# Optimization experiments

Hardware: AMD Instinct MI355X
Metric: run time of the kernel (lower is better)

## Reference

```python
import jax, jax.numpy as jnp
import numpy as np

N_NODES = 100000
N_EDGES = 3200000
N_GRAPHS = 2048
MOL_DIM = 78
HID = 32
OUT = 128
N_LAYERS = 5
BN_EPS = 1e-5


def setup_inputs() -> dict:
    key = jax.random.key(0)
    ks = jax.random.split(key, 16)
    x = jax.random.normal(ks[0], (N_NODES, MOL_DIM), dtype=jnp.float32)
    edge_index = jax.random.randint(ks[1], (2, N_EDGES), 0, N_NODES, dtype=jnp.int32)
    batch = jnp.sort(jax.random.randint(ks[2], (N_NODES,), 0, N_GRAPHS, dtype=jnp.int32))
    def lin(k, fan_in, shape):
        b = 1.0 / np.sqrt(fan_in)
        return jax.random.uniform(k, shape, jnp.float32, -b, b)
    # layer 0 MLP (78 -> 32 -> 32)
    w1_0 = lin(ks[3], MOL_DIM, (MOL_DIM, HID))
    b1_0 = lin(ks[4], MOL_DIM, (HID,))
    w2_0 = lin(ks[5], HID, (HID, HID))
    b2_0 = lin(ks[6], HID, (HID,))
    # layers 1..4 MLPs (32 -> 32 -> 32), stacked
    w1 = lin(ks[7], HID, (N_LAYERS - 1, HID, HID))
    b1 = lin(ks[8], HID, (N_LAYERS - 1, HID))
    w2 = lin(ks[9], HID, (N_LAYERS - 1, HID, HID))
    b2 = lin(ks[10], HID, (N_LAYERS - 1, HID))
    # BatchNorm affine params per layer
    gamma = jnp.ones((N_LAYERS, HID), jnp.float32)
    beta = jnp.zeros((N_LAYERS, HID), jnp.float32)
    # final fc (32 -> 128)
    fc_w = lin(ks[11], HID, (HID, OUT))
    fc_b = lin(ks[12], HID, (OUT,))
    return {"x": x, "edge_index": edge_index, "batch": batch,
            "w1_0": w1_0, "b1_0": b1_0, "w2_0": w2_0, "b2_0": b2_0,
            "w1": w1, "b1": b1, "w2": w2, "b2": b2,
            "gamma": gamma, "beta": beta, "fc_w": fc_w, "fc_b": fc_b}


def _gin_layer(x, src, dst, W1, B1, W2, B2, g, bt):
    # GIN aggregation: (1+eps)*x + sum_{j in N(i)} x_j, eps = 0
    agg = x + jax.ops.segment_sum(x[src], dst, num_segments=N_NODES)
    h = jnp.maximum(agg @ W1 + B1, 0.0)   # Linear + ReLU
    h = h @ W2 + B2                        # Linear
    h = jnp.maximum(h, 0.0)                # outer act before BN
    mean = jnp.mean(h, axis=0)
    var = jnp.mean(jnp.square(h - mean), axis=0)  # biased (training BN)
    return (h - mean) * jax.lax.rsqrt(var + BN_EPS) * g + bt


def reference(x, edge_index, batch, w1_0, b1_0, w2_0, b2_0,
              w1, b1, w2, b2, gamma, beta, fc_w, fc_b):
    src, dst = edge_index[0], edge_index[1]
    h = _gin_layer(x, src, dst, w1_0, b1_0, w2_0, b2_0, gamma[0], beta[0])
    for i in range(N_LAYERS - 1):
        h = _gin_layer(h, src, dst, w1[i], b1[i], w2[i], b2[i],
                       gamma[i + 1], beta[i + 1])
    pooled = jax.ops.segment_sum(h, batch, num_segments=N_GRAPHS)  # [G, HID]
    out = jnp.maximum(pooled @ fc_w + fc_b, 0.0)  # dropout is identity in eval
    return out
```

## Files before the change

### kernel.cpp

```cpp
#include <hip/hip_runtime.h>

#define N_NODES 100000
#define N_EDGES 3200000
#define N_GRAPHS 2048
#define MOL 78
#define HID 32
#define OUTD 128
#define BN_EPS 1e-5f

#define NBUCK ((N_NODES + 255) / 256)
#define BCAP2 9216
#define EPB 4096
#define P1_BLOCKS ((N_EDGES + EPB - 1) / EPB)

#define NPH 4
#define CPL_BLOCKS (N_NODES / (8 * NPH))

#define NCOPY 64


__global__ __launch_bounds__(256) void part1_kernel(const int* __restrict__ src,
                                                    const int* __restrict__ dst,
                                                    int* __restrict__ gcur,
                                                    int* __restrict__ staging) {
    __shared__ int hist[NBUCK];
    __shared__ int lofs[NBUCK];
    __shared__ int lcur[NBUCK];
    __shared__ int gb[NBUCK];
    __shared__ int pk[EPB];
    __shared__ unsigned short bkt[EPB];
    __shared__ int sc[256];
    const int t = threadIdx.x;
    const int base = blockIdx.x * EPB;
    const int nedge = min(EPB, N_EDGES - base);

    for (int i = t; i < NBUCK; i += 256) hist[i] = 0;
    __syncthreads();
    for (int i = t; i < nedge; i += 256) atomicAdd(&hist[dst[base + i] >> 8], 1);
    __syncthreads();

    int a0 = (2 * t < NBUCK) ? hist[2 * t] : 0;
    int a1 = (2 * t + 1 < NBUCK) ? hist[2 * t + 1] : 0;
    int tot = a0 + a1;
    sc[t] = tot;
    __syncthreads();
    for (int off = 1; off < 256; off <<= 1) {
        int add = (t >= off) ? sc[t - off] : 0;
        __syncthreads();
        sc[t] += add;
        __syncthreads();
    }
    int excl = sc[t] - tot;
    if (2 * t < NBUCK) { lofs[2 * t] = excl; lcur[2 * t] = excl; }
    if (2 * t + 1 < NBUCK) { lofs[2 * t + 1] = excl + a0; lcur[2 * t + 1] = excl + a0; }
    __syncthreads();

    for (int i = t; i < nedge; i += 256) {
        int d = dst[base + i];
        int s = src[base + i];
        int b = d >> 8;
        int p = atomicAdd(&lcur[b], 1);
        pk[p] = (s << 8) | (d & 255);
        bkt[p] = (unsigned short)b;
    }
    __syncthreads();

    for (int b = t; b < NBUCK; b += 256) {
        int c = lcur[b] - lofs[b];
        gb[b] = c ? atomicAdd(&gcur[b], c) : 0;
    }
    __syncthreads();

    for (int i = t; i < nedge; i += 256) {
        int b = bkt[i];
        staging[(size_t)b * BCAP2 + gb[b] + (i - lofs[b])] = pk[i];
    }
}

__global__ void csrbase_kernel(const int* __restrict__ gcur, int* __restrict__ bbase,
                               int* __restrict__ row_start) {
    int t = threadIdx.x;
    int a0 = (2 * t < NBUCK) ? gcur[2 * t] : 0;
    int a1 = (2 * t + 1 < NBUCK) ? gcur[2 * t + 1] : 0;
    int tot = a0 + a1;
    __shared__ int sc[256];
    sc[t] = tot;
    __syncthreads();
    for (int off = 1; off < 256; off <<= 1) {
        int add = (t >= off) ? sc[t - off] : 0;
        __syncthreads();
        sc[t] += add;
        __syncthreads();
    }
    int excl = sc[t] - tot;
    if (2 * t < NBUCK) bbase[2 * t] = excl;
    if (2 * t + 1 < NBUCK) bbase[2 * t + 1] = excl + a0;
    if (t == 0) row_start[N_NODES] = N_EDGES;
}

__global__ __launch_bounds__(256) void part2_kernel(const int* __restrict__ gcur,
                                                    const int* __restrict__ bbase,
                                                    const int* __restrict__ staging,
                                                    int* __restrict__ row_start,
                                                    int* __restrict__ csr,
                                                    float* __restrict__ degf) {
    int b = blockIdx.x, t = threadIdx.x;
    __shared__ int ldeg[256];
    __shared__ int lex[256];
    __shared__ int sc[256];
    ldeg[t] = 0;
    __syncthreads();
    int cnt = gcur[b];
    int base = bbase[b];
    const int* sp = staging + (size_t)b * BCAP2;
    for (int i = t; i < cnt; i += 256) atomicAdd(&ldeg[sp[i] & 255], 1);
    __syncthreads();
    int v = ldeg[t];
    sc[t] = v;
    __syncthreads();
    for (int off = 1; off < 256; off <<= 1) {
        int add = (t >= off) ? sc[t - off] : 0;
        __syncthreads();
        sc[t] += add;
        __syncthreads();
    }
    int excl = sc[t] - v;
    int node = b * 256 + t;
    if (node < N_NODES) {
        row_start[node] = base + excl;
        degf[node] = 1.0f + (float)v;
    }
    lex[t] = base + excl;
    __syncthreads();
    for (int i = t; i < cnt; i += 256) {
        int pk = sp[i];
        int p = atomicAdd(&lex[pk & 255], 1);
        csr[p] = pk >> 8;
    }
}


__global__ void gcnt_kernel(const int* __restrict__ batch, int* __restrict__ cnt) {
    int g = blockIdx.x * blockDim.x + threadIdx.x;
    if (g >= N_GRAPHS) return;
    auto lb = [&](int key) {
        int lo = 0, hi = N_NODES;
        while (lo < hi) {
            int mid = (lo + hi) >> 1;
            if (batch[mid] < key) lo = mid + 1; else hi = mid;
        }
        return lo;
    };
    cnt[g] = lb(g + 1) - lb(g);
}


__global__ __launch_bounds__(256) void proj78_kernel(const float* __restrict__ in,
                                                     const float* __restrict__ W1,
                                                     float* __restrict__ y) {
    __shared__ float w1s[MOL * HID];
    for (int i = threadIdx.x; i < MOL * HID; i += 256) w1s[i] = W1[i];
    __syncthreads();
    const int node = blockIdx.x * 256 + threadIdx.x;
    if (node >= N_NODES) return;
    const float* row = in + (size_t)node * MOL;
    float acc[HID];
#pragma unroll
    for (int j = 0; j < HID; j++) acc[j] = 0.f;
    const float4* w1v = (const float4*)w1s;
    for (int k = 0; k < MOL; k++) {
        float xv = row[k];
#pragma unroll
        for (int q = 0; q < 8; q++) {
            float4 wv = w1v[k * 8 + q];
            acc[4 * q + 0] = fmaf(xv, wv.x, acc[4 * q + 0]);
            acc[4 * q + 1] = fmaf(xv, wv.y, acc[4 * q + 1]);
            acc[4 * q + 2] = fmaf(xv, wv.z, acc[4 * q + 2]);
            acc[4 * q + 3] = fmaf(xv, wv.w, acc[4 * q + 3]);
        }
    }
    float4* o = (float4*)(y + (size_t)node * HID);
#pragma unroll
    for (int q = 0; q < 8; q++)
        o[q] = make_float4(acc[4 * q], acc[4 * q + 1], acc[4 * q + 2], acc[4 * q + 3]);
}


__global__ __launch_bounds__(256) void agg_kernel(const float* __restrict__ y,
                                                  const int* __restrict__ rs,
                                                  const int* __restrict__ csr,
                                                  float* __restrict__ agg) {
    int gt = blockIdx.x * blockDim.x + threadIdx.x;
    int node = gt >> 5;
    if (node >= N_NODES) return;
    int hl = threadIdx.x & 31;
    int s = hl >> 3;
    int q = hl & 7;
    const float4* rows = (const float4*)y;
    float4 acc = (s == 0) ? rows[(size_t)node * 8 + q] : make_float4(0.f, 0.f, 0.f, 0.f);
    float4 acc2 = make_float4(0.f, 0.f, 0.f, 0.f);
    int e0 = rs[node], e1 = rs[node + 1];
    int k = e0 + s;
    for (; k + 12 < e1; k += 16) {
        int j0 = csr[k];
        int j1 = csr[k + 4];
        int j2 = csr[k + 8];
        int j3 = csr[k + 12];
        float4 v0 = rows[(size_t)j0 * 8 + q];
        float4 v1 = rows[(size_t)j1 * 8 + q];
        float4 v2 = rows[(size_t)j2 * 8 + q];
        float4 v3 = rows[(size_t)j3 * 8 + q];
        acc.x += v0.x + v1.x;
        acc.y += v0.y + v1.y;
        acc.z += v0.z + v1.z;
        acc.w += v0.w + v1.w;
        acc2.x += v2.x + v3.x;
        acc2.y += v2.y + v3.y;
        acc2.z += v2.z + v3.z;
        acc2.w += v2.w + v3.w;
    }
    for (; k < e1; k += 4) {
        int j = csr[k];
        float4 v = rows[(size_t)j * 8 + q];
        acc.x += v.x;
        acc.y += v.y;
        acc.z += v.z;
        acc.w += v.w;
    }
    acc.x += acc2.x;
    acc.y += acc2.y;
    acc.z += acc2.z;
    acc.w += acc2.w;
#pragma unroll
    for (int m = 8; m <= 16; m <<= 1) {
        acc.x += __shfl_xor(acc.x, m, 32);
        acc.y += __shfl_xor(acc.y, m, 32);
        acc.z += __shfl_xor(acc.z, m, 32);
        acc.w += __shfl_xor(acc.w, m, 32);
    }
    if (s == 0) ((float4*)agg)[(size_t)node * 8 + q] = acc;
}


__global__ __launch_bounds__(256) void mlp2cpl_kernel(const float* __restrict__ agg,
                                                      const float* __restrict__ B1,
                                                      const float* __restrict__ W2,
                                                      const float* __restrict__ B2,
                                                      float* __restrict__ out,
                                                      float* __restrict__ sums) {
    __shared__ float ldsv[8][NPH][HID];
    __shared__ float ssum[64];
    const int t = threadIdx.x;
    const int hw = t >> 5;
    const int c = t & 31;
    if (t < 64) ssum[t] = 0.f;
    float w2col[32];
#pragma unroll
    for (int k = 0; k < 32; k++) w2col[k] = W2[k * 32 + c];
    const float b1c = B1[c], b2c = B2[c];
    const int n0 = (blockIdx.x * 8 + hw) * NPH;
#pragma unroll
    for (int u = 0; u < NPH; u++) {
        float v = fmaxf(agg[(size_t)(n0 + u) * 32 + c] + b1c, 0.f);
        ldsv[hw][u][c] = v;
    }
    __syncthreads();
    float sl = 0.f, sq = 0.f;
#pragma unroll
    for (int u = 0; u < NPH; u++) {
        float h = b2c;
        const float4* vv4 = (const float4*)&ldsv[hw][u][0];
#pragma unroll
        for (int q = 0; q < 8; q++) {
            float4 vv = vv4[q];
            h = fmaf(vv.x, w2col[4 * q + 0], h);
            h = fmaf(vv.y, w2col[4 * q + 1], h);
            h = fmaf(vv.z, w2col[4 * q + 2], h);
            h = fmaf(vv.w, w2col[4 * q + 3], h);
        }
        h = fmaxf(h, 0.f);
        out[(size_t)(n0 + u) * 32 + c] = h;
        sl += h;
        sq += h * h;
    }
    atomicAdd(&ssum[c], sl);
    atomicAdd(&ssum[32 + c], sq);
    __syncthreads();
    if (t < 64) atomicAdd(&sums[(blockIdx.x & (NCOPY - 1)) * 64 + t], ssum[t]);
}


template <bool LAST>
__global__ __launch_bounds__(256) void fusedmlp_kernel(
    const float* __restrict__ aggh, const float* __restrict__ degf,
    const float* __restrict__ scsh_prev, const float* __restrict__ B1,
    const float* __restrict__ W1, const float* __restrict__ W2, const float* __restrict__ B2,
    float* __restrict__ out, float* __restrict__ sums, const int* __restrict__ batch,
    float* __restrict__ pooledraw) {
    __shared__ float ldsu[8][NPH][HID];
    __shared__ float ldsv[8][HID];
    __shared__ float ssum[64];
    const int t = threadIdx.x;
    const int hw = t >> 5;
    const int c = t & 31;
    if (t < 64) ssum[t] = 0.f;
    float w1col[32], w2col[32];
#pragma unroll
    for (int k = 0; k < 32; k++) {
        w1col[k] = W1[k * 32 + c];
        w2col[k] = W2[k * 32 + c];
    }
    const float scv = scsh_prev[c], shv = scsh_prev[HID + c];
    const float b1c = B1[c], b2c = B2[c];
    const int n0 = (blockIdx.x * 8 + hw) * NPH;
#pragma unroll
    for (int u = 0; u < NPH; u++) {
        int n = n0 + u;
        float cdeg = degf[n];
        ldsu[hw][u][c] = fmaf(aggh[(size_t)n * 32 + c], scv, cdeg * shv);
    }
    __syncthreads();
    float sl = 0.f, sq = 0.f;
#pragma unroll
    for (int u = 0; u < NPH; u++) {
        const int n = n0 + u;
        float tv = b1c;
        const float4* uu4 = (const float4*)&ldsu[hw][u][0];
#pragma unroll
        for (int q = 0; q < 8; q++) {
            float4 uu = uu4[q];
            tv = fmaf(uu.x, w1col[4 * q + 0], tv);
            tv = fmaf(uu.y, w1col[4 * q + 1], tv);
            tv = fmaf(uu.z, w1col[4 * q + 2], tv);
            tv = fmaf(uu.w, w1col[4 * q + 3], tv);
        }
        tv = fmaxf(tv, 0.f);
        ldsv[hw][c] = tv;
        float h = b2c;
        const float4* vv4 = (const float4*)&ldsv[hw][0];
#pragma unroll
        for (int q = 0; q < 8; q++) {
            float4 vv = vv4[q];
            h = fmaf(vv.x, w2col[4 * q + 0], h);
            h = fmaf(vv.y, w2col[4 * q + 1], h);
            h = fmaf(vv.z, w2col[4 * q + 2], h);
            h = fmaf(vv.w, w2col[4 * q + 3], h);
        }
        h = fmaxf(h, 0.f);
        if (LAST) {
            atomicAdd(&pooledraw[batch[n] * HID + c], h);
        } else {
            out[(size_t)n * 32 + c] = h;
        }
        sl += h;
        sq += h * h;
    }
    atomicAdd(&ssum[c], sl);
    atomicAdd(&ssum[32 + c], sq);
    __syncthreads();
    if (t < 64) atomicAdd(&sums[(blockIdx.x & (NCOPY - 1)) * 64 + t], ssum[t]);
}


__global__ void bnfin_kernel(const float* __restrict__ sums, const float* __restrict__ g,
                             const float* __restrict__ bt, float* __restrict__ scsh) {
    __shared__ float red[64];
    int t = threadIdx.x;
    if (t < 64) {
        float acc = 0.f;
#pragma unroll 8
        for (int k = 0; k < NCOPY; k++) acc += sums[k * 64 + t];
        red[t] = acc;
    }
    __syncthreads();
    if (t < HID) {
        float m = red[t] * (1.0f / N_NODES);
        float var = red[HID + t] * (1.0f / N_NODES) - m * m;
        var = fmaxf(var, 0.f);
        float sc = g[t] * rsqrtf(var + BN_EPS);
        scsh[t] = sc;
        scsh[HID + t] = bt[t] - m * sc;
    }
}


__global__ void fc_kernel(const float* __restrict__ praw, const int* __restrict__ cnt,
                          const float* __restrict__ scsh4, const float* __restrict__ fcw,
                          const float* __restrict__ fcb, float* __restrict__ out) {
    __shared__ float w[HID * OUTD];
    __shared__ float aff[2 * HID];
    for (int i = threadIdx.x; i < HID * OUTD; i += 256) w[i] = fcw[i];
    if (threadIdx.x < 2 * HID) aff[threadIdx.x] = scsh4[threadIdx.x];
    __syncthreads();
    int idx = blockIdx.x * 256 + threadIdx.x;
    if (idx >= N_GRAPHS * OUTD) return;
    int g = idx >> 7;
    int o = idx & 127;
    float cg = (float)cnt[g];
    float acc = fcb[o];
#pragma unroll
    for (int k = 0; k < HID; k++) {
        float paff = fmaf(praw[g * HID + k], aff[k], cg * aff[HID + k]);
        acc = fmaf(paff, w[k * OUTD + o], acc);
    }
    out[idx] = fmaxf(acc, 0.f);
}


extern "C" void kernel_launch(void* const* d_in, const int* in_sizes, int n_in,
                              void* d_out, int out_size, void* d_ws, size_t ws_size,
                              hipStream_t stream) {
    const float* x = (const float*)d_in[0];
    const int* ei = (const int*)d_in[1];
    const int* batch = (const int*)d_in[2];
    const float* w1_0 = (const float*)d_in[3];
    const float* b1_0 = (const float*)d_in[4];
    const float* w2_0 = (const float*)d_in[5];
    const float* b2_0 = (const float*)d_in[6];
    const float* w1 = (const float*)d_in[7];
    const float* b1 = (const float*)d_in[8];
    const float* w2 = (const float*)d_in[9];
    const float* b2 = (const float*)d_in[10];
    const float* gamma = (const float*)d_in[11];
    const float* beta = (const float*)d_in[12];
    const float* fc_w = (const float*)d_in[13];
    const float* fc_b = (const float*)d_in[14];
    float* out = (float*)d_out;

    const int* e_src = ei;
    const int* e_dst = ei + N_EDGES;

    char* ws = (char*)d_ws;
    size_t off = 0;
    auto alloc = [&](size_t n) {
        void* p = ws + off;
        off += (n + 255) & ~(size_t)255;
        return p;
    };
    int* row_start = (int*)alloc((size_t)(N_NODES + 1) * 4);
    int* csr = (int*)alloc((size_t)N_EDGES * 4);
    int* bbase = (int*)alloc((size_t)NBUCK * 4);
    int* staging = (int*)alloc((size_t)NBUCK * BCAP2 * 4);
    float* ybuf = (float*)alloc((size_t)N_NODES * HID * 4);
    float* aggb = (float*)alloc((size_t)N_NODES * HID * 4);
    float* hbuf = (float*)alloc((size_t)N_NODES * HID * 4);
    float* degf = (float*)alloc((size_t)N_NODES * 4);
    float* scsh = (float*)alloc(5 * 2 * HID * 4);
    int* cnt = (int*)alloc((size_t)N_GRAPHS * 4);
    size_t zero_base = off;
    int* gcur = (int*)alloc((size_t)NBUCK * 4);
    float* bnsums = (float*)alloc((size_t)5 * NCOPY * 64 * 4);
    float* pooled = (float*)alloc((size_t)N_GRAPHS * HID * 4);
    size_t zero_len = off - zero_base;

    hipMemsetAsync(ws + zero_base, 0, zero_len, stream);

    part1_kernel<<<P1_BLOCKS, 256, 0, stream>>>(e_src, e_dst, gcur, staging);
    csrbase_kernel<<<1, 256, 0, stream>>>(gcur, bbase, row_start);
    part2_kernel<<<NBUCK, 256, 0, stream>>>(gcur, bbase, staging, row_start, csr, degf);
    gcnt_kernel<<<(N_GRAPHS + 255) / 256, 256, 0, stream>>>(batch, cnt);

    const int nodeBlocks = (N_NODES + 255) / 256;
    const int aggBlocks = (N_NODES * 32 + 255) / 256;

    proj78_kernel<<<nodeBlocks, 256, 0, stream>>>(x, w1_0, ybuf);
    agg_kernel<<<aggBlocks, 256, 0, stream>>>(ybuf, row_start, csr, aggb);
    mlp2cpl_kernel<<<CPL_BLOCKS, 256, 0, stream>>>(aggb, b1_0, w2_0, b2_0, hbuf, bnsums);
    bnfin_kernel<<<1, 64, 0, stream>>>(bnsums, gamma, beta, scsh);

    for (int l = 1; l < 5; l++) {
        int i = l - 1;
        agg_kernel<<<aggBlocks, 256, 0, stream>>>(hbuf, row_start, csr, aggb);
        if (l < 4) {
            fusedmlp_kernel<false><<<CPL_BLOCKS, 256, 0, stream>>>(
                aggb, degf, scsh + (l - 1) * 2 * HID, b1 + (size_t)i * HID,
                w1 + (size_t)i * HID * HID, w2 + (size_t)i * HID * HID, b2 + (size_t)i * HID,
                hbuf, bnsums + (size_t)l * NCOPY * 64, nullptr, nullptr);
        } else {
            fusedmlp_kernel<true><<<CPL_BLOCKS, 256, 0, stream>>>(
                aggb, degf, scsh + (l - 1) * 2 * HID, b1 + (size_t)i * HID,
                w1 + (size_t)i * HID * HID, w2 + (size_t)i * HID * HID, b2 + (size_t)i * HID,
                nullptr, bnsums + (size_t)l * NCOPY * 64, batch, pooled);
        }
        bnfin_kernel<<<1, 64, 0, stream>>>(bnsums + (size_t)l * NCOPY * 64, gamma + l * HID,
                                           beta + l * HID, scsh + l * 2 * HID);
    }

    fc_kernel<<<(N_GRAPHS * OUTD + 255) / 256, 256, 0, stream>>>(
        pooled, cnt, scsh + 4 * 2 * HID, fc_w, fc_b, out);
}
```

Before: 506.5 us.

## Store node features as fp16 to halve gather traffic in aggregation

Node feature buffers fed to the neighbor aggregation (the projected layer-0 features and the per-layer hidden outputs) are now stored as packed fp16 instead of fp32. The aggregation kernel gathers 16-byte packs covering 8 halves each and accumulates in fp32. It is restructured so that 4 lanes cover a row and 8 edge slots run in parallel, with a deeper shuffle reduction. This is meant to halve the bytes moved by the random-access gather over 3.2M edges, which dominates the runtime. In exchange it rounds the stored features to half precision, adding error that may affect accuracy tolerance.

```diff
diff --git a/kernel.cpp b/kernel.cpp
--- a/kernel.cpp
+++ b/kernel.cpp
@@ -1,4 +1,5 @@
 #include <hip/hip_runtime.h>
+#include <hip/hip_fp16.h>
 
 #define N_NODES 100000
 #define N_EDGES 3200000
@@ -17,6 +18,19 @@
 #define CPL_BLOCKS (N_NODES / (8 * NPH))
 
 #define NCOPY 64
+
+__device__ inline unsigned int pkh2(float a, float b) {
+    __half2 h = __halves2half2(__float2half_rn(a), __float2half_rn(b));
+    return *(unsigned int*)&h;
+}
+__device__ inline float hlo(unsigned int v) {
+    __half2 h = *(__half2*)&v;
+    return __low2float(h);
+}
+__device__ inline float hhi(unsigned int v) {
+    __half2 h = *(__half2*)&v;
+    return __high2float(h);
+}
 
 
 __global__ __launch_bounds__(256) void part1_kernel(const int* __restrict__ src,
@@ -157,7 +171,7 @@
 
 __global__ __launch_bounds__(256) void proj78_kernel(const float* __restrict__ in,
                                                      const float* __restrict__ W1,
-                                                     float* __restrict__ y) {
+                                                     unsigned int* __restrict__ y) {
     __shared__ float w1s[MOL * HID];
     for (int i = threadIdx.x; i < MOL * HID; i += 256) w1s[i] = W1[i];
     __syncthreads();
@@ -179,14 +193,20 @@
             acc[4 * q + 3] = fmaf(xv, wv.w, acc[4 * q + 3]);
         }
     }
-    float4* o = (float4*)(y + (size_t)node * HID);
-#pragma unroll
-    for (int q = 0; q < 8; q++)
-        o[q] = make_float4(acc[4 * q], acc[4 * q + 1], acc[4 * q + 2], acc[4 * q + 3]);
-}
-
-
-__global__ __launch_bounds__(256) void agg_kernel(const float* __restrict__ y,
+    uint4* o = (uint4*)(y + (size_t)node * 16);
+#pragma unroll
+    for (int g = 0; g < 4; g++) {
+        uint4 u;
+        u.x = pkh2(acc[8 * g + 0], acc[8 * g + 1]);
+        u.y = pkh2(acc[8 * g + 2], acc[8 * g + 3]);
+        u.z = pkh2(acc[8 * g + 4], acc[8 * g + 5]);
+        u.w = pkh2(acc[8 * g + 6], acc[8 * g + 7]);
+        o[g] = u;
+    }
+}
+
+
+__global__ __launch_bounds__(256) void agg_kernel(const unsigned int* __restrict__ y,
                                                   const int* __restrict__ rs,
                                                   const int* __restrict__ csr,
                                                   float* __restrict__ agg) {
@@ -194,51 +214,50 @@
     int node = gt >> 5;
     if (node >= N_NODES) return;
     int hl = threadIdx.x & 31;
-    int s = hl >> 3;
-    int q = hl & 7;
-    const float4* rows = (const float4*)y;
-    float4 acc = (s == 0) ? rows[(size_t)node * 8 + q] : make_float4(0.f, 0.f, 0.f, 0.f);
-    float4 acc2 = make_float4(0.f, 0.f, 0.f, 0.f);
+    int s = hl >> 2;
+    int q = hl & 3;
+    const uint4* rows = (const uint4*)y;
+    float acc[8];
+#pragma unroll
+    for (int i = 0; i < 8; i++) acc[i] = 0.f;
+    if (s == 0) {
+        uint4 u = rows[(size_t)node * 4 + q];
+        acc[0] = hlo(u.x); acc[1] = hhi(u.x);
+        acc[2] = hlo(u.y); acc[3] = hhi(u.y);
+        acc[4] = hlo(u.z); acc[5] = hhi(u.z);
+        acc[6] = hlo(u.w); acc[7] = hhi(u.w);
+    }
     int e0 = rs[node], e1 = rs[node + 1];
     int k = e0 + s;
-    for (; k + 12 < e1; k += 16) {
-        int j0 = csr[k];
-        int j1 = csr[k + 4];
-        int j2 = csr[k + 8];
-        int j3 = csr[k + 12];
-        float4 v0 = rows[(size_t)j0 * 8 + q];
-        float4 v1 = rows[(size_t)j1 * 8 + q];
-        float4 v2 = rows[(size_t)j2 * 8 + q];
-        float4 v3 = rows[(size_t)j3 * 8 + q];
-        acc.x += v0.x + v1.x;
-        acc.y += v0.y + v1.y;
-        acc.z += v0.z + v1.z;
-        acc.w += v0.w + v1.w;
-        acc2.x += v2.x + v3.x;
-        acc2.y += v2.y + v3.y;
-        acc2.z += v2.z + v3.z;
-        acc2.w += v2.w + v3.w;
-    }
-    for (; k < e1; k += 4) {
-        int j = csr[k];
-        float4 v = rows[(size_t)j * 8 + q];
-        acc.x += v.x;
-        acc.y += v.y;
-        acc.z += v.z;
-        acc.w += v.w;
-    }
-    acc.x += acc2.x;
-    acc.y += acc2.y;
-    acc.z += acc2.z;
-    acc.w += acc2.w;
-#pragma unroll
-    for (int m = 8; m <= 16; m <<= 1) {
-        acc.x += __shfl_xor(acc.x, m, 32);
-        acc.y += __shfl_xor(acc.y, m, 32);
-        acc.z += __shfl_xor(acc.z, m, 32);
-        acc.w += __shfl_xor(acc.w, m, 32);
-    }
-    if (s == 0) ((float4*)agg)[(size_t)node * 8 + q] = acc;
+    for (; k + 8 < e1; k += 16) {
+        uint4 a = rows[(size_t)csr[k] * 4 + q];
+        uint4 b = rows[(size_t)csr[k + 8] * 4 + q];
+        acc[0] += hlo(a.x) + hlo(b.x);
+        acc[1] += hhi(a.x) + hhi(b.x);
+        acc[2] += hlo(a.y) + hlo(b.y);
+        acc[3] += hhi(a.y) + hhi(b.y);
+        acc[4] += hlo(a.z) + hlo(b.z);
+        acc[5] += hhi(a.z) + hhi(b.z);
+        acc[6] += hlo(a.w) + hlo(b.w);
+        acc[7] += hhi(a.w) + hhi(b.w);
+    }
+    if (k < e1) {
+        uint4 a = rows[(size_t)csr[k] * 4 + q];
+        acc[0] += hlo(a.x); acc[1] += hhi(a.x);
+        acc[2] += hlo(a.y); acc[3] += hhi(a.y);
+        acc[4] += hlo(a.z); acc[5] += hhi(a.z);
+        acc[6] += hlo(a.w); acc[7] += hhi(a.w);
+    }
+#pragma unroll
+    for (int m = 4; m <= 16; m <<= 1) {
+#pragma unroll
+        for (int i = 0; i < 8; i++) acc[i] += __shfl_xor(acc[i], m, 32);
+    }
+    if (s == 0) {
+        float4* o = (float4*)(agg + (size_t)node * HID + q * 8);
+        o[0] = make_float4(acc[0], acc[1], acc[2], acc[3]);
+        o[1] = make_float4(acc[4], acc[5], acc[6], acc[7]);
+    }
 }
 
 
@@ -246,7 +265,7 @@
                                                       const float* __restrict__ B1,
                                                       const float* __restrict__ W2,
                                                       const float* __restrict__ B2,
-                                                      float* __restrict__ out,
+                                                      __half* __restrict__ out,
                                                       float* __restrict__ sums) {
     __shared__ float ldsv[8][NPH][HID];
     __shared__ float ssum[64];
@@ -279,7 +298,7 @@
             h = fmaf(vv.w, w2col[4 * q + 3], h);
         }
         h = fmaxf(h, 0.f);
-        out[(size_t)(n0 + u) * 32 + c] = h;
+        out[(size_t)(n0 + u) * 32 + c] = __float2half_rn(h);
         sl += h;
         sq += h * h;
     }
@@ -295,7 +314,7 @@
     const float* __restrict__ aggh, const float* __restrict__ degf,
     const float* __restrict__ scsh_prev, const float* __restrict__ B1,
     const float* __restrict__ W1, const float* __restrict__ W2, const float* __restrict__ B2,
-    float* __restrict__ out, float* __restrict__ sums, const int* __restrict__ batch,
+    __half* __restrict__ out, float* __restrict__ sums, const int* __restrict__ batch,
     float* __restrict__ pooledraw) {
     __shared__ float ldsu[8][NPH][HID];
     __shared__ float ldsv[8][HID];
@@ -350,7 +369,7 @@
         if (LAST) {
             atomicAdd(&pooledraw[batch[n] * HID + c], h);
         } else {
-            out[(size_t)n * 32 + c] = h;
+            out[(size_t)n * 32 + c] = __float2half_rn(h);
         }
         sl += h;
         sq += h * h;
@@ -441,9 +460,9 @@
     int* csr = (int*)alloc((size_t)N_EDGES * 4);
     int* bbase = (int*)alloc((size_t)NBUCK * 4);
     int* staging = (int*)alloc((size_t)NBUCK * BCAP2 * 4);
-    float* ybuf = (float*)alloc((size_t)N_NODES * HID * 4);
+    unsigned int* ybuf = (unsigned int*)alloc((size_t)N_NODES * 16 * 4);
     float* aggb = (float*)alloc((size_t)N_NODES * HID * 4);
-    float* hbuf = (float*)alloc((size_t)N_NODES * HID * 4);
+    __half* hbuf = (__half*)alloc((size_t)N_NODES * HID * 2);
     float* degf = (float*)alloc((size_t)N_NODES * 4);
     float* scsh = (float*)alloc(5 * 2 * HID * 4);
     int* cnt = (int*)alloc((size_t)N_GRAPHS * 4);
@@ -470,7 +489,8 @@
 
     for (int l = 1; l < 5; l++) {
         int i = l - 1;
-        agg_kernel<<<aggBlocks, 256, 0, stream>>>(hbuf, row_start, csr, aggb);
+        agg_kernel<<<aggBlocks, 256, 0, stream>>>((const unsigned int*)hbuf, row_start, csr,
+                                                  aggb);
         if (l < 4) {
             fusedmlp_kernel<false><<<CPL_BLOCKS, 256, 0, stream>>>(
                 aggb, degf, scsh + (l - 1) * 2 * HID, b1 + (size_t)i * HID,
```

New measurement: 424.4 us. 1.19x faster.
